# Kernel optimization log

Measured on AMD Instinct MI355X. Metric: run time of the kernel, lower is better.

## Reference

```python
import jax, jax.numpy as jnp
import numpy as np

DIM = 1024
N_HEADS = 16
SCALE = (DIM // N_HEADS) ** (-0.5)


def setup_inputs() -> dict:
    key = jax.random.key(0)
    kq, kk, kv = jax.random.split(key, 3)
    shape = (4, 16, 2048, 64)  # [B, H, N, Dh]
    q = jax.random.normal(kq, shape, dtype=jnp.float32)
    k = jax.random.normal(kk, shape, dtype=jnp.float32)
    v = jax.random.normal(kv, shape, dtype=jnp.float32)
    return {"q": q, "k": k, "v": v}


def reference(q, k, v):
    # Faithful translation of the torch module, INCLUDING its einsum output
    # subscripts: the second einsum is 'bhnm,bhmd->bhmd' (sums over n, keeps m),
    # exactly as written in the source.
    scores = jnp.einsum('bhnd,bhmd->bhnm', q, k) * SCALE  # [B,H,N,M]
    scores = jax.nn.softmax(scores, axis=-1)
    out = jnp.einsum('bhnm,bhmd->bhmd', scores, v)  # [B,H,M,Dh]
    return out
```

## Files before the change

kernel.cpp:

```cpp
#include <hip/hip_runtime.h>
#include <cstdint>
#include <cstddef>

#define B_    4
#define H_    16
#define N_    2048
#define D_    64
#define BH_   (B_*H_)
#define SCALE 0.125f
#define QSCL  0.18033688011f

#define P_    256
#define T_    128
#define NT    (N_/T_)
#define NP    (N_/P_)
#define TILEB 16384
#define BHB   (NT*TILEB)

typedef __attribute__((ext_vector_type(8))) short bf16x8;
typedef __attribute__((ext_vector_type(4))) float f32x4;

#if __has_builtin(__builtin_amdgcn_exp2f)
#define EXP2(x) __builtin_amdgcn_exp2f(x)
#else
#define EXP2(x) exp2f(x)
#endif

__device__ __forceinline__ short f2bf(float f) {
    union { float f; unsigned u; } x; x.f = f;
    unsigned r = x.u + 0x7FFF + ((x.u >> 16) & 1);
    return (short)(r >> 16);
}

__device__ __forceinline__ size_t swz(int row, int cc) {
    return ((size_t)(row >> 7) * TILEB) + ((row & 127) << 7) + ((cc ^ (row & 7)) << 4);
}

__global__ __launch_bounds__(512)
void mha_convert(const float* __restrict__ q, const float* __restrict__ k,
                 char* __restrict__ qk)
{
    const int gid = blockIdx.x * 512 + threadIdx.x;
    const int half = BH_ * N_ * 8;
    const bool isq = gid < half;
    const float* src = isq ? q : k;
    const float scl = isq ? QSCL : 1.0f;
    char* dst = qk + (isq ? 0 : (size_t)BH_ * BHB);
    const int id = isq ? gid : gid - half;
    const int bh  = id >> 14;
    const int row = (id >> 3) & 2047;
    const int cc  = id & 7;
    const float* p = src + ((size_t)bh * N_ + row) * D_ + cc * 8;
    float4 a = *(const float4*)p;
    float4 b = *(const float4*)(p + 4);
    bf16x8 o;
    o[0] = f2bf(a.x * scl); o[1] = f2bf(a.y * scl);
    o[2] = f2bf(a.z * scl); o[3] = f2bf(a.w * scl);
    o[4] = f2bf(b.x * scl); o[5] = f2bf(b.y * scl);
    o[6] = f2bf(b.z * scl); o[7] = f2bf(b.w * scl);
    *(bf16x8*)(dst + (size_t)bh * BHB + swz(row, cc)) = o;
}

__global__ __launch_bounds__(512)
void mha_rowsum2(const char* __restrict__ qk, float* __restrict__ rinv)
{
    __shared__ __align__(16) char KT[TILEB];

    const int t = threadIdx.x, w = t >> 6, l = t & 63;
    const int wid = (blockIdx.x & 7) * 64 + (blockIdx.x >> 3);
    const int bh = wid / NP, rb = wid % NP;

    const char* Qp = qk + (size_t)bh * BHB;
    const char* Kp = qk + (size_t)BH_ * BHB + (size_t)bh * BHB;

    bf16x8 af[2][2];
    #pragma unroll
    for (int rg = 0; rg < 2; ++rg)
        #pragma unroll
        for (int kh = 0; kh < 2; ++kh) {
            int row = rb * P_ + w * 32 + rg * 16 + (l & 15);
            af[rg][kh] = *(const bf16x8*)(Qp + swz(row, kh * 4 + (l >> 4)));
        }

    float rs[2][4] = {};

    for (int ct = 0; ct < NT; ++ct) {
        __syncthreads();
        const char* src = Kp + (size_t)ct * TILEB;
        *(bf16x8*)(KT + t * 16)        = *(const bf16x8*)(src + t * 16);
        *(bf16x8*)(KT + 8192 + t * 16) = *(const bf16x8*)(src + 8192 + t * 16);
        __syncthreads();

        #pragma unroll
        for (int cj = 0; cj < 8; ++cj) {
            const int krow = cj * 16 + (l & 15);
            const int kb = (krow & 127) << 7;
            bf16x8 b0 = *(const bf16x8*)(KT + kb + (((l >> 4) ^ (krow & 7)) << 4));
            bf16x8 b1 = *(const bf16x8*)(KT + kb + (((4 + (l >> 4)) ^ (krow & 7)) << 4));
            #pragma unroll
            for (int rg = 0; rg < 2; ++rg) {
                f32x4 c = {0.f, 0.f, 0.f, 0.f};
                c = __builtin_amdgcn_mfma_f32_16x16x32_bf16(af[rg][0], b0, c, 0, 0, 0);
                c = __builtin_amdgcn_mfma_f32_16x16x32_bf16(af[rg][1], b1, c, 0, 0, 0);
                rs[rg][0] += EXP2(c[0]);
                rs[rg][1] += EXP2(c[1]);
                rs[rg][2] += EXP2(c[2]);
                rs[rg][3] += EXP2(c[3]);
            }
        }
    }

    #pragma unroll
    for (int rg = 0; rg < 2; ++rg)
        #pragma unroll
        for (int i = 0; i < 4; ++i) {
            rs[rg][i] += __shfl_xor(rs[rg][i], 1);
            rs[rg][i] += __shfl_xor(rs[rg][i], 2);
            rs[rg][i] += __shfl_xor(rs[rg][i], 4);
            rs[rg][i] += __shfl_xor(rs[rg][i], 8);
        }
    if ((l & 15) == 0) {
        #pragma unroll
        for (int rg = 0; rg < 2; ++rg) {
            const int rbase = rb * P_ + w * 32 + rg * 16 + (l >> 4) * 4;
            #pragma unroll
            for (int i = 0; i < 4; ++i)
                rinv[(size_t)bh * N_ + rbase + i] = 1.0f / rs[rg][i];
        }
    }
}

__global__ __launch_bounds__(512)
void mha_colsum2(const char* __restrict__ qk, const float* __restrict__ rinv,
                 const float* __restrict__ v, float* __restrict__ out)
{
    __shared__ __align__(16) char QT[TILEB];
    __shared__ float rv[T_];
    __shared__ float cs[P_];

    const int t = threadIdx.x, w = t >> 6, l = t & 63;
    const int wid = (blockIdx.x & 7) * 64 + (blockIdx.x >> 3);
    const int bh = wid / NP, cb = wid % NP;

    const char* Qp = qk + (size_t)bh * BHB;
    const char* Kp = qk + (size_t)BH_ * BHB + (size_t)bh * BHB;
    const float* Rg = rinv + (size_t)bh * N_;

    bf16x8 kf[2][2];
    #pragma unroll
    for (int rg = 0; rg < 2; ++rg)
        #pragma unroll
        for (int kh = 0; kh < 2; ++kh) {
            int col = cb * P_ + w * 32 + rg * 16 + (l & 15);
            kf[rg][kh] = *(const bf16x8*)(Kp + swz(col, kh * 4 + (l >> 4)));
        }

    float ca[2] = {0.f, 0.f};

    for (int rt = 0; rt < NT; ++rt) {
        __syncthreads();
        const char* src = Qp + (size_t)rt * TILEB;
        *(bf16x8*)(QT + t * 16)        = *(const bf16x8*)(src + t * 16);
        *(bf16x8*)(QT + 8192 + t * 16) = *(const bf16x8*)(src + 8192 + t * 16);
        if (t < T_) rv[t] = Rg[rt * T_ + t];
        __syncthreads();

        #pragma unroll
        for (int rj = 0; rj < 8; ++rj) {
            const int qr = rj * 16 + (l & 15);
            const int qb = (qr & 127) << 7;
            bf16x8 a0 = *(const bf16x8*)(QT + qb + (((l >> 4) ^ (qr & 7)) << 4));
            bf16x8 a1 = *(const bf16x8*)(QT + qb + (((4 + (l >> 4)) ^ (qr & 7)) << 4));
            float4 r4 = *(const float4*)&rv[rj * 16 + (l >> 4) * 4];
            #pragma unroll
            for (int rg = 0; rg < 2; ++rg) {
                f32x4 c = {0.f, 0.f, 0.f, 0.f};
                c = __builtin_amdgcn_mfma_f32_16x16x32_bf16(a0, kf[rg][0], c, 0, 0, 0);
                c = __builtin_amdgcn_mfma_f32_16x16x32_bf16(a1, kf[rg][1], c, 0, 0, 0);
                ca[rg] += EXP2(c[0]) * r4.x + EXP2(c[1]) * r4.y
                        + EXP2(c[2]) * r4.z + EXP2(c[3]) * r4.w;
            }
        }
    }

    #pragma unroll
    for (int rg = 0; rg < 2; ++rg) {
        ca[rg] += __shfl_xor(ca[rg], 16);
        ca[rg] += __shfl_xor(ca[rg], 32);
    }
    if (l < 16) { cs[w * 32 + l] = ca[0]; cs[w * 32 + 16 + l] = ca[1]; }
    __syncthreads();

    const float4* Vg = (const float4*)(v + ((size_t)bh * N_ + cb * P_) * D_);
    float4* Og = (float4*)(out + ((size_t)bh * N_ + cb * P_) * D_);
    #pragma unroll
    for (int i = 0; i < 8; ++i) {
        int id = i * 512 + t;
        float s = cs[id >> 4];
        float4 vv = Vg[id];
        float4 o; o.x = vv.x * s; o.y = vv.y * s; o.z = vv.z * s; o.w = vv.w * s;
        Og[id] = o;
    }
}

#define FTS 128
#define FNT 16

__device__ __forceinline__ bf16x8 cvt8(const float* p) {
    float4 a = *(const float4*)p;
    float4 b = *(const float4*)(p + 4);
    bf16x8 r;
    r[0] = f2bf(a.x); r[1] = f2bf(a.y); r[2] = f2bf(a.z); r[3] = f2bf(a.w);
    r[4] = f2bf(b.x); r[5] = f2bf(b.y); r[6] = f2bf(b.z); r[7] = f2bf(b.w);
    return r;
}
__device__ __forceinline__ void fstage(char* lds, const float* src, int t) {
    #pragma unroll
    for (int i = 0; i < 2; ++i) {
        int ch = i * 512 + t, r = ch >> 3, cc = ch & 7;
        bf16x8 v = cvt8(src + (size_t)r * D_ + cc * 8);
        *(bf16x8*)(lds + r * 128 + ((cc ^ (r & 7)) << 4)) = v;
    }
}
__device__ __forceinline__ bf16x8 fread(const char* lds, int row, int cc) {
    return *(const bf16x8*)(lds + row * 128 + ((cc ^ (row & 7)) << 4));
}

__global__ __launch_bounds__(512)
void mha_rowsum_fb(const float* __restrict__ q, const float* __restrict__ k,
                   float* __restrict__ rinv)
{
    __shared__ __align__(16) char KT[FTS * 128];
    const int t = threadIdx.x, w = t >> 6, l = t & 63;
    const int bh = blockIdx.x / FNT, rb = blockIdx.x % FNT;
    const float* Qg = q + (size_t)bh * N_ * D_;
    const float* Kg = k + (size_t)bh * N_ * D_;
    const int qrow = rb * FTS + w * 16 + (l & 15);
    bf16x8 af[2];
    #pragma unroll
    for (int kh = 0; kh < 2; ++kh)
        af[kh] = cvt8(Qg + (size_t)qrow * D_ + kh * 32 + (l >> 4) * 8);
    float rs[4] = {0.f, 0.f, 0.f, 0.f};
    for (int ct = 0; ct < FNT; ++ct) {
        __syncthreads();
        fstage(KT, Kg + (size_t)ct * FTS * D_, t);
        __syncthreads();
        #pragma unroll
        for (int cj = 0; cj < 8; ++cj) {
            const int krow = cj * 16 + (l & 15);
            f32x4 c = {0.f, 0.f, 0.f, 0.f};
            #pragma unroll
            for (int kh = 0; kh < 2; ++kh)
                c = __builtin_amdgcn_mfma_f32_16x16x32_bf16(af[kh], fread(KT, krow, kh * 4 + (l >> 4)), c, 0, 0, 0);
            rs[0] += __expf(c[0] * SCALE); rs[1] += __expf(c[1] * SCALE);
            rs[2] += __expf(c[2] * SCALE); rs[3] += __expf(c[3] * SCALE);
        }
    }
    #pragma unroll
    for (int i = 0; i < 4; ++i) {
        rs[i] += __shfl_xor(rs[i], 1); rs[i] += __shfl_xor(rs[i], 2);
        rs[i] += __shfl_xor(rs[i], 4); rs[i] += __shfl_xor(rs[i], 8);
    }
    if ((l & 15) == 0) {
        const int rbase = rb * FTS + w * 16 + (l >> 4) * 4;
        #pragma unroll
        for (int i = 0; i < 4; ++i)
            rinv[(size_t)bh * N_ + rbase + i] = 1.0f / rs[i];
    }
}

__global__ __launch_bounds__(512)
void mha_colsum_fb(const float* __restrict__ q, const float* __restrict__ k,
                   const float* __restrict__ v, const float* __restrict__ rinv,
                   float* __restrict__ out)
{
    __shared__ __align__(16) char QT[FTS * 128];
    __shared__ float rv[FTS];
    __shared__ float cs[FTS];
    const int t = threadIdx.x, w = t >> 6, l = t & 63;
    const int bh = blockIdx.x / FNT, cb = blockIdx.x % FNT;
    const float* Qg = q + (size_t)bh * N_ * D_;
    const float* Kg = k + (size_t)bh * N_ * D_;
    const float* Rg = rinv + (size_t)bh * N_;
    const int kcol = cb * FTS + w * 16 + (l & 15);
    bf16x8 kf[2];
    #pragma unroll
    for (int kh = 0; kh < 2; ++kh)
        kf[kh] = cvt8(Kg + (size_t)kcol * D_ + kh * 32 + (l >> 4) * 8);
    float ca = 0.f;
    for (int rt = 0; rt < FNT; ++rt) {
        __syncthreads();
        fstage(QT, Qg + (size_t)rt * FTS * D_, t);
        if (t < FTS) rv[t] = Rg[rt * FTS + t];
        __syncthreads();
        #pragma unroll
        for (int rj = 0; rj < 8; ++rj) {
            const int qr = rj * 16 + (l & 15);
            f32x4 c = {0.f, 0.f, 0.f, 0.f};
            #pragma unroll
            for (int kh = 0; kh < 2; ++kh)
                c = __builtin_amdgcn_mfma_f32_16x16x32_bf16(fread(QT, qr, kh * 4 + (l >> 4)), kf[kh], c, 0, 0, 0);
            float4 r4 = *(const float4*)&rv[rj * 16 + (l >> 4) * 4];
            ca += __expf(c[0] * SCALE) * r4.x + __expf(c[1] * SCALE) * r4.y
                + __expf(c[2] * SCALE) * r4.z + __expf(c[3] * SCALE) * r4.w;
        }
    }
    ca += __shfl_xor(ca, 16); ca += __shfl_xor(ca, 32);
    if (l < 16) cs[w * 16 + l] = ca;
    __syncthreads();
    const float4* Vg = (const float4*)(v + (size_t)bh * N_ * D_ + (size_t)cb * FTS * D_);
    float4* Og = (float4*)(out + (size_t)bh * N_ * D_ + (size_t)cb * FTS * D_);
    #pragma unroll
    for (int i = 0; i < 4; ++i) {
        int id = i * 512 + t;
        float s = cs[id >> 4];
        float4 vv = Vg[id];
        float4 o; o.x = vv.x * s; o.y = vv.y * s; o.z = vv.z * s; o.w = vv.w * s;
        Og[id] = o;
    }
}

extern "C" void kernel_launch(void* const* d_in, const int* in_sizes, int n_in,
                              void* d_out, int out_size, void* d_ws, size_t ws_size,
                              hipStream_t stream)
{
    const float* q = (const float*)d_in[0];
    const float* k = (const float*)d_in[1];
    const float* v = (const float*)d_in[2];
    float* out = (float*)d_out;

    const size_t qkBytes = (size_t)2 * BH_ * BHB;
    const size_t need = qkBytes + (size_t)BH_ * N_ * 4;

    if (ws_size >= need) {
        char* qk = (char*)d_ws;
        float* rinv = (float*)(qk + qkBytes);
        mha_convert<<<dim3(2 * BH_ * N_ * 8 / 512), dim3(512), 0, stream>>>(q, k, qk);
        mha_rowsum2<<<dim3(BH_ * NP), dim3(512), 0, stream>>>(qk, rinv);
        mha_colsum2<<<dim3(BH_ * NP), dim3(512), 0, stream>>>(qk, rinv, v, out);
    } else {
        float* rinv = (float*)d_ws;
        mha_rowsum_fb<<<dim3(BH_ * FNT), dim3(512), 0, stream>>>(q, k, rinv);
        mha_colsum_fb<<<dim3(BH_ * FNT), dim3(512), 0, stream>>>(q, k, v, rinv, out);
    }
}
```

Before: 108.4 us.

## Double-buffer K/Q tiles via direct global-to-LDS loads in rowsum/colsum kernels

Both pass kernels now stage their 16KB bf16 tiles into two LDS buffers with global_load_lds, prefetching two tiles ahead and waiting with explicit vmcnt counters plus raw s_barrier. This overlaps the global fetch of the next tile with MFMA/exp2 work on the current one and removes the register round trip of the old copy loop. It also precomputes the swizzled LDS offsets per lane. The colsum kernel gives each wave its own copy of the row-inverse vector so it can be loaded the same way. The cost is double the LDS footprint, and correctness now depends on hand-written waitcnt counts.

```diff
diff --git a/kernel.cpp b/kernel.cpp
--- a/kernel.cpp
+++ b/kernel.cpp
@@ -26,6 +26,10 @@
 #define EXP2(x) exp2f(x)
 #endif
 
+#define BARRIER() do { asm volatile("" ::: "memory"); \
+                       __builtin_amdgcn_s_barrier();  \
+                       asm volatile("" ::: "memory"); } while (0)
+
 __device__ __forceinline__ short f2bf(float f) {
     union { float f; unsigned u; } x; x.f = f;
     unsigned r = x.u + 0x7FFF + ((x.u >> 16) & 1);
@@ -34,6 +38,17 @@
 
 __device__ __forceinline__ size_t swz(int row, int cc) {
     return ((size_t)(row >> 7) * TILEB) + ((row & 127) << 7) + ((cc ^ (row & 7)) << 4);
+}
+
+__device__ __forceinline__ void gload_lds16(const char* g, char* l) {
+    __builtin_amdgcn_global_load_lds(
+        (const __attribute__((address_space(1))) void*)g,
+        (__attribute__((address_space(3))) void*)l, 16, 0, 0);
+}
+__device__ __forceinline__ void gload_lds4(const float* g, float* l) {
+    __builtin_amdgcn_global_load_lds(
+        (const __attribute__((address_space(1))) void*)g,
+        (__attribute__((address_space(3))) void*)l, 4, 0, 0);
 }
 
 __global__ __launch_bounds__(512)
@@ -62,9 +77,9 @@
 }
 
 __global__ __launch_bounds__(512)
-void mha_rowsum2(const char* __restrict__ qk, float* __restrict__ rinv)
-{
-    __shared__ __align__(16) char KT[TILEB];
+void mha_rowsum6(const char* __restrict__ qk, float* __restrict__ rinv)
+{
+    __shared__ __align__(16) char KT[2][TILEB];
 
     const int t = threadIdx.x, w = t >> 6, l = t & 63;
     const int wid = (blockIdx.x & 7) * 64 + (blockIdx.x >> 3);
@@ -77,26 +92,31 @@
     #pragma unroll
     for (int rg = 0; rg < 2; ++rg)
         #pragma unroll
-        for (int kh = 0; kh < 2; ++kh) {
-            int row = rb * P_ + w * 32 + rg * 16 + (l & 15);
-            af[rg][kh] = *(const bf16x8*)(Qp + swz(row, kh * 4 + (l >> 4)));
-        }
+        for (int kh = 0; kh < 2; ++kh)
+            af[rg][kh] = *(const bf16x8*)(Qp + swz(rb * P_ + w * 32 + rg * 16 + (l & 15),
+                                                   kh * 4 + (l >> 4)));
+    #pragma unroll
+    for (int rg = 0; rg < 2; ++rg)
+        #pragma unroll
+        for (int kh = 0; kh < 2; ++kh)
+            asm volatile("" :: "v"(af[rg][kh]));
+
+    const int lb0 = (l & 15) * 128 + (((l >> 4) ^ (l & 7)) << 4);
+    const int lb1 = (l & 15) * 128 + (((4 + (l >> 4)) ^ (l & 7)) << 4);
+    const int t16 = t * 16;
 
     float rs[2][4] = {};
 
-    for (int ct = 0; ct < NT; ++ct) {
-        __syncthreads();
+    auto STAGE = [&](int ct, int buf) {
         const char* src = Kp + (size_t)ct * TILEB;
-        *(bf16x8*)(KT + t * 16)        = *(const bf16x8*)(src + t * 16);
-        *(bf16x8*)(KT + 8192 + t * 16) = *(const bf16x8*)(src + 8192 + t * 16);
-        __syncthreads();
-
+        gload_lds16(src + t16,        KT[buf] + t16);
+        gload_lds16(src + 8192 + t16, KT[buf] + 8192 + t16);
+    };
+    auto COMPUTE = [&](const char* kt) {
         #pragma unroll
         for (int cj = 0; cj < 8; ++cj) {
-            const int krow = cj * 16 + (l & 15);
-            const int kb = (krow & 127) << 7;
-            bf16x8 b0 = *(const bf16x8*)(KT + kb + (((l >> 4) ^ (krow & 7)) << 4));
-            bf16x8 b1 = *(const bf16x8*)(KT + kb + (((4 + (l >> 4)) ^ (krow & 7)) << 4));
+            bf16x8 b0 = *(const bf16x8*)(kt + lb0 + cj * 2048);
+            bf16x8 b1 = *(const bf16x8*)(kt + lb1 + cj * 2048);
             #pragma unroll
             for (int rg = 0; rg < 2; ++rg) {
                 f32x4 c = {0.f, 0.f, 0.f, 0.f};
@@ -108,7 +128,24 @@
                 rs[rg][3] += EXP2(c[3]);
             }
         }
-    }
+    };
+
+    STAGE(0, 0);
+    STAGE(1, 1);
+    #pragma unroll 1
+    for (int ct = 0; ct < NT - 2; ++ct) {
+        asm volatile("s_waitcnt vmcnt(2)" ::: "memory");
+        BARRIER();
+        COMPUTE(KT[ct & 1]);
+        BARRIER();
+        STAGE(ct + 2, ct & 1);
+    }
+    asm volatile("s_waitcnt vmcnt(2)" ::: "memory");
+    BARRIER();
+    COMPUTE(KT[(NT - 2) & 1]);
+    asm volatile("s_waitcnt vmcnt(0)" ::: "memory");
+    BARRIER();
+    COMPUTE(KT[(NT - 1) & 1]);
 
     #pragma unroll
     for (int rg = 0; rg < 2; ++rg)
@@ -131,11 +168,11 @@
 }
 
 __global__ __launch_bounds__(512)
-void mha_colsum2(const char* __restrict__ qk, const float* __restrict__ rinv,
+void mha_colsum6(const char* __restrict__ qk, const float* __restrict__ rinv,
                  const float* __restrict__ v, float* __restrict__ out)
 {
-    __shared__ __align__(16) char QT[TILEB];
-    __shared__ float rv[T_];
+    __shared__ __align__(16) char QT[2][TILEB];
+    __shared__ float rvw[2][8][T_];
     __shared__ float cs[P_];
 
     const int t = threadIdx.x, w = t >> 6, l = t & 63;
@@ -150,28 +187,36 @@
     #pragma unroll
     for (int rg = 0; rg < 2; ++rg)
         #pragma unroll
-        for (int kh = 0; kh < 2; ++kh) {
-            int col = cb * P_ + w * 32 + rg * 16 + (l & 15);
-            kf[rg][kh] = *(const bf16x8*)(Kp + swz(col, kh * 4 + (l >> 4)));
-        }
+        for (int kh = 0; kh < 2; ++kh)
+            kf[rg][kh] = *(const bf16x8*)(Kp + swz(cb * P_ + w * 32 + rg * 16 + (l & 15),
+                                                    kh * 4 + (l >> 4)));
+    #pragma unroll
+    for (int rg = 0; rg < 2; ++rg)
+        #pragma unroll
+        for (int kh = 0; kh < 2; ++kh)
+            asm volatile("" :: "v"(kf[rg][kh]));
+
+    const int lb0 = (l & 15) * 128 + (((l >> 4) ^ (l & 7)) << 4);
+    const int lb1 = (l & 15) * 128 + (((4 + (l >> 4)) ^ (l & 7)) << 4);
+    const int t16 = t * 16;
 
     float ca[2] = {0.f, 0.f};
 
-    for (int rt = 0; rt < NT; ++rt) {
-        __syncthreads();
+    auto STAGE = [&](int rt, int buf) {
         const char* src = Qp + (size_t)rt * TILEB;
-        *(bf16x8*)(QT + t * 16)        = *(const bf16x8*)(src + t * 16);
-        *(bf16x8*)(QT + 8192 + t * 16) = *(const bf16x8*)(src + 8192 + t * 16);
-        if (t < T_) rv[t] = Rg[rt * T_ + t];
-        __syncthreads();
-
+        gload_lds16(src + t16,        QT[buf] + t16);
+        gload_lds16(src + 8192 + t16, QT[buf] + 8192 + t16);
+        const float* rsrc = Rg + rt * T_;
+        float* rdst = &rvw[buf][w][0];
+        gload_lds4(rsrc + l,      rdst + l);
+        gload_lds4(rsrc + 64 + l, rdst + 64 + l);
+    };
+    auto COMPUTE = [&](const char* qt, const float* rvb) {
         #pragma unroll
         for (int rj = 0; rj < 8; ++rj) {
-            const int qr = rj * 16 + (l & 15);
-            const int qb = (qr & 127) << 7;
-            bf16x8 a0 = *(const bf16x8*)(QT + qb + (((l >> 4) ^ (qr & 7)) << 4));
-            bf16x8 a1 = *(const bf16x8*)(QT + qb + (((4 + (l >> 4)) ^ (qr & 7)) << 4));
-            float4 r4 = *(const float4*)&rv[rj * 16 + (l >> 4) * 4];
+            bf16x8 a0 = *(const bf16x8*)(qt + lb0 + rj * 2048);
+            bf16x8 a1 = *(const bf16x8*)(qt + lb1 + rj * 2048);
+            float4 r4 = *(const float4*)(rvb + rj * 16 + (l >> 4) * 4);
             #pragma unroll
             for (int rg = 0; rg < 2; ++rg) {
                 f32x4 c = {0.f, 0.f, 0.f, 0.f};
@@ -181,7 +226,24 @@
                         + EXP2(c[2]) * r4.z + EXP2(c[3]) * r4.w;
             }
         }
-    }
+    };
+
+    STAGE(0, 0);
+    STAGE(1, 1);
+    #pragma unroll 1
+    for (int rt = 0; rt < NT - 2; ++rt) {
+        asm volatile("s_waitcnt vmcnt(4)" ::: "memory");
+        BARRIER();
+        COMPUTE(QT[rt & 1], &rvw[rt & 1][w][0]);
+        BARRIER();
+        STAGE(rt + 2, rt & 1);
+    }
+    asm volatile("s_waitcnt vmcnt(4)" ::: "memory");
+    BARRIER();
+    COMPUTE(QT[(NT - 2) & 1], &rvw[(NT - 2) & 1][w][0]);
+    asm volatile("s_waitcnt vmcnt(0)" ::: "memory");
+    BARRIER();
+    COMPUTE(QT[(NT - 1) & 1], &rvw[(NT - 1) & 1][w][0]);
 
     #pragma unroll
     for (int rg = 0; rg < 2; ++rg) {
@@ -336,8 +398,8 @@
         char* qk = (char*)d_ws;
         float* rinv = (float*)(qk + qkBytes);
         mha_convert<<<dim3(2 * BH_ * N_ * 8 / 512), dim3(512), 0, stream>>>(q, k, qk);
-        mha_rowsum2<<<dim3(BH_ * NP), dim3(512), 0, stream>>>(qk, rinv);
-        mha_colsum2<<<dim3(BH_ * NP), dim3(512), 0, stream>>>(qk, rinv, v, out);
+        mha_rowsum6<<<dim3(BH_ * NP), dim3(512), 0, stream>>>(qk, rinv);
+        mha_colsum6<<<dim3(BH_ * NP), dim3(512), 0, stream>>>(qk, rinv, v, out);
     } else {
         float* rinv = (float*)d_ws;
         mha_rowsum_fb<<<dim3(BH_ * FNT), dim3(512), 0, stream>>>(q, k, rinv);
```

Result: no change. 108.6 us (+0.1%).
